# Kernel optimization log

Measured on AMD Instinct MI355X. Metric: run time of the kernel, lower is better.

The kernel has to match this reference:

```python
import jax, jax.numpy as jnp
import numpy as np

NUM_HEAD = 32
SIZE_PER_HEAD = 64
START_LEN = 4080
SEQ_LEN = 4096
STEPS = SEQ_LEN - START_LEN  # 16 unrolled decode steps
BATCH = 32
SCALE = 0.125  # hard-coded in the original (1/sqrt(64))


def setup_inputs() -> dict:
    key = jax.random.key(0)
    ks = jax.random.split(key, 7)
    B, H, D, S = BATCH, NUM_HEAD, SIZE_PER_HEAD, SEQ_LEN
    xavier = float(np.sqrt(6.0 / (D + D)))  # xavier_uniform_ bound for [D, D] fan
    return {
        "x": jax.random.normal(ks[0], (B, H, 1, D), dtype=jnp.float32),
        "k": jax.random.normal(ks[1], (B, H, S, D), dtype=jnp.float32),
        "v": jax.random.normal(ks[2], (B, H, S, D), dtype=jnp.float32),
        "wq": jax.random.uniform(ks[3], (H, D, D), jnp.float32, -xavier, xavier),
        "wk": jax.random.uniform(ks[4], (H, D, D), jnp.float32, -xavier, xavier),
        "wv": jax.random.uniform(ks[5], (H, D, D), jnp.float32, -xavier, xavier),
        "wo": jax.random.uniform(ks[6], (H, D, D), jnp.float32, -xavier, xavier),
    }


def _decode(x, k, v, wq, wk, wv, wo):
    # x: [B, H, 1, D]; k, v: [B, H, S, D]; weights: [H, D, D]
    def step(carry, _):
        x, k, v, gen_id = carry
        q = jnp.einsum("bhod,hde->bhoe", x, wq)            # [B, H, 1, D]
        k_new = jnp.einsum("bhod,hde->bhoe", x, wk)        # [B, H, 1, D]
        v_new = jnp.einsum("bhod,hde->bhoe", x, wv)
        k = jax.lax.dynamic_update_slice_in_dim(k, k_new, gen_id, axis=2)
        v = jax.lax.dynamic_update_slice_in_dim(v, v_new, gen_id, axis=2)
        # scores over the FULL cache (no mask), matching torch softmax over dim=3
        attn = jnp.einsum("bhsd,bhod->bhos", k, q) * SCALE  # [B, H, 1, S]
        attn = jax.nn.softmax(attn, axis=-1)
        x = jnp.einsum("bhos,bhsd->bhod", attn, v)          # [B, H, 1, D]
        x = jnp.einsum("bhod,hde->bhoe", x, wo)
        return (x, k, v, gen_id + 1), None

    (x, k, v, _), _ = jax.lax.scan(step, (x, k, v, jnp.int32(START_LEN)), None, length=STEPS)
    return x


def reference(x, k, v, wq, wk, wv, wo):
    return _decode(x, k, v, wq, wk, wv, wo)
```

## Files before the change

### kernel.cpp

```cpp
#include <hip/hip_runtime.h>
#include <hip/hip_fp16.h>
#include <math.h>

#define BATCH   32
#define NHEAD   32
#define DIM     64
#define SEQ     4096
#define START   4080
#define NSTEPS  16
#define SCALE   0.125f

typedef float fvec4 __attribute__((ext_vector_type(4)));

template <bool USE_WS>
__launch_bounds__(256, 6)
__global__ void attn_unroll_kernel(const float* __restrict__ x_in,
                                   const float* __restrict__ k_in,
                                   const float* __restrict__ v_in,
                                   const float* __restrict__ wq,
                                   const float* __restrict__ wk,
                                   const float* __restrict__ wv,
                                   const float* __restrict__ wo,
                                   float* __restrict__ out,
                                   __half* __restrict__ kh_ws,
                                   __half* __restrict__ vh_ws)
{
    const int bid = blockIdx.x;
    const int h   = bid & (NHEAD - 1);
    const int tid = threadIdx.x;

    __shared__ float s_scores[SEQ];
    __shared__ float s_kext[NSTEPS][DIM];
    __shared__ float s_vext[NSTEPS][DIM];
    __shared__ float s_x[DIM];
    __shared__ float s_q[DIM];
    __shared__ float s_attn[DIM];
    __shared__ float s_red[4][DIM];
    __shared__ float s_wred[4];

    const float* __restrict__ K  = k_in + (size_t)bid * SEQ * DIM;
    const float* __restrict__ V  = v_in + (size_t)bid * SEQ * DIM;
    const float* __restrict__ Wq = wq + (size_t)h * DIM * DIM;
    const float* __restrict__ Wk = wk + (size_t)h * DIM * DIM;
    const float* __restrict__ Wv = wv + (size_t)h * DIM * DIM;
    const float* __restrict__ Wo = wo + (size_t)h * DIM * DIM;
    __half* __restrict__ Kh = USE_WS ? kh_ws + (size_t)bid * START * DIM : nullptr;
    __half* __restrict__ Vh = USE_WS ? vh_ws + (size_t)bid * START * DIM : nullptr;

    if (tid < DIM) s_x[tid] = x_in[(size_t)bid * DIM + tid];
    for (int i = tid; i < NSTEPS * DIM; i += 256) {
        (&s_kext[0][0])[i] = K[(size_t)START * DIM + i];
        (&s_vext[0][0])[i] = V[(size_t)START * DIM + i];
    }
    __syncthreads();

    auto project = [&](const float* in_vec, const float* __restrict__ W,
                       float* out_vec) {
        const int e = tid & 63;
        const int g = tid >> 6;
        float p = 0.f;
        #pragma unroll
        for (int dd = 0; dd < 16; ++dd) {
            const int d0 = g * 16 + dd;
            p += in_vec[d0] * W[d0 * 64 + e];
        }
        s_red[g][e] = p;
        __syncthreads();
        if (tid < 64)
            out_vec[tid] = s_red[0][tid] + s_red[1][tid]
                         + s_red[2][tid] + s_red[3][tid];
        __syncthreads();
    };

    const int c    = tid & 15;
    const int sr   = tid >> 4;
    const int c8   = tid & 7;
    const int rg   = tid >> 3;
    const int wave = tid >> 6;

    auto qk_f32 = [&]() {
        const float q0 = s_q[c * 4 + 0], q1 = s_q[c * 4 + 1];
        const float q2 = s_q[c * 4 + 2], q3 = s_q[c * 4 + 3];
        const fvec4* __restrict__ K4 = (const fvec4*)K;
        for (int it = 0; it < START / 16; ++it) {
            const int s = it * 16 + sr;
            const fvec4 kv = __builtin_nontemporal_load(&K4[s * 16 + c]);
            if (USE_WS) {
                __half2* dst = (__half2*)(Kh + (size_t)s * DIM + c * 4);
                dst[0] = __floats2half2_rn(kv.x, kv.y);
                dst[1] = __floats2half2_rn(kv.z, kv.w);
            }
            float p = kv.x * q0 + kv.y * q1 + kv.z * q2 + kv.w * q3;
            p += __shfl_xor(p, 1);
            p += __shfl_xor(p, 2);
            p += __shfl_xor(p, 4);
            p += __shfl_xor(p, 8);
            if (c == 0) s_scores[s] = p;
        }
        {
            const int s = START + sr;
            const float* kr = s_kext[sr];
            float p = kr[c * 4 + 0] * q0 + kr[c * 4 + 1] * q1
                    + kr[c * 4 + 2] * q2 + kr[c * 4 + 3] * q3;
            p += __shfl_xor(p, 1);
            p += __shfl_xor(p, 2);
            p += __shfl_xor(p, 4);
            p += __shfl_xor(p, 8);
            if (c == 0) s_scores[s] = p;
        }
    };

    auto qk_h = [&]() {
        float qv[8];
        #pragma unroll
        for (int j = 0; j < 8; ++j) qv[j] = s_q[c8 * 8 + j];
        const fvec4* __restrict__ Kh4 = (const fvec4*)Kh;
        auto row = [&](int s) {
            fvec4 raw = Kh4[(size_t)s * 8 + c8];
            const __half2* hp = (const __half2*)&raw;
            float p = 0.f;
            #pragma unroll
            for (int j = 0; j < 4; ++j) {
                const float2 f = __half22float2(hp[j]);
                p += f.x * qv[2 * j] + f.y * qv[2 * j + 1];
            }
            p += __shfl_xor(p, 1);
            p += __shfl_xor(p, 2);
            p += __shfl_xor(p, 4);
            if (c8 == 0) s_scores[s] = p;
        };
        for (int it = 0; it < 127; ++it)
            row(it * 32 + rg);
        if (rg < 16) {
            row(4064 + rg);
            const float* kr = s_kext[rg];
            float p = 0.f;
            #pragma unroll
            for (int j = 0; j < 8; ++j) p += kr[c8 * 8 + j] * qv[j];
            p += __shfl_xor(p, 1);
            p += __shfl_xor(p, 2);
            p += __shfl_xor(p, 4);
            if (c8 == 0) s_scores[START + rg] = p;
        }
    };

    auto pv_f32 = [&](float inv_total) {
        float ax = 0.f, ay = 0.f, az = 0.f, aw = 0.f;
        const fvec4* __restrict__ V4 = (const fvec4*)V;
        for (int it = 0; it < START / 16; ++it) {
            const int s = it * 16 + sr;
            const fvec4 vv = __builtin_nontemporal_load(&V4[s * 16 + c]);
            if (USE_WS) {
                __half2* dst = (__half2*)(Vh + (size_t)s * DIM + c * 4);
                dst[0] = __floats2half2_rn(vv.x, vv.y);
                dst[1] = __floats2half2_rn(vv.z, vv.w);
            }
            const float a = s_scores[s];
            ax += a * vv.x; ay += a * vv.y; az += a * vv.z; aw += a * vv.w;
        }
        {
            const int s = START + sr;
            const float a  = s_scores[s];
            const float* vr = s_vext[sr];
            ax += a * vr[c * 4 + 0]; ay += a * vr[c * 4 + 1];
            az += a * vr[c * 4 + 2]; aw += a * vr[c * 4 + 3];
        }
        ax += __shfl_xor(ax, 16); ax += __shfl_xor(ax, 32);
        ay += __shfl_xor(ay, 16); ay += __shfl_xor(ay, 32);
        az += __shfl_xor(az, 16); az += __shfl_xor(az, 32);
        aw += __shfl_xor(aw, 16); aw += __shfl_xor(aw, 32);
        if ((tid & 63) < 16) {
            s_red[wave][c * 4 + 0] = ax;
            s_red[wave][c * 4 + 1] = ay;
            s_red[wave][c * 4 + 2] = az;
            s_red[wave][c * 4 + 3] = aw;
        }
        __syncthreads();
        if (tid < 64)
            s_attn[tid] = (s_red[0][tid] + s_red[1][tid]
                         + s_red[2][tid] + s_red[3][tid]) * inv_total;
        __syncthreads();
    };

    auto pv_h = [&](float inv_total) {
        float a[8];
        #pragma unroll
        for (int j = 0; j < 8; ++j) a[j] = 0.f;
        const fvec4* __restrict__ Vh4 = (const fvec4*)Vh;
        auto row = [&](int s) {
            const float w = s_scores[s];
            fvec4 raw = Vh4[(size_t)s * 8 + c8];
            const __half2* hp = (const __half2*)&raw;
            #pragma unroll
            for (int j = 0; j < 4; ++j) {
                const float2 f = __half22float2(hp[j]);
                a[2 * j + 0] += w * f.x;
                a[2 * j + 1] += w * f.y;
            }
        };
        for (int it = 0; it < 127; ++it)
            row(it * 32 + rg);
        if (rg < 16) {
            row(4064 + rg);
            const float w = s_scores[START + rg];
            const float* vr = s_vext[rg];
            #pragma unroll
            for (int j = 0; j < 8; ++j) a[j] += w * vr[c8 * 8 + j];
        }
        #pragma unroll
        for (int j = 0; j < 8; ++j) {
            a[j] += __shfl_xor(a[j], 8);
            a[j] += __shfl_xor(a[j], 16);
            a[j] += __shfl_xor(a[j], 32);
        }
        if ((tid & 63) < 8) {
            #pragma unroll
            for (int j = 0; j < 8; ++j) s_red[wave][c8 * 8 + j] = a[j];
        }
        __syncthreads();
        if (tid < 64)
            s_attn[tid] = (s_red[0][tid] + s_red[1][tid]
                         + s_red[2][tid] + s_red[3][tid]) * inv_total;
        __syncthreads();
    };

    for (int step = 0; step < NSTEPS; ++step) {
        project(s_x, Wq, s_q);
        project(s_x, Wk, s_kext[step]);
        project(s_x, Wv, s_vext[step]);
        if (tid < 64) s_q[tid] *= SCALE;
        __syncthreads();

        if (USE_WS && step > 0) qk_h(); else qk_f32();
        __syncthreads();

        float lmax = -1e30f;
        #pragma unroll
        for (int i = 0; i < 16; ++i)
            lmax = fmaxf(lmax, s_scores[tid + i * 256]);
        #pragma unroll
        for (int off = 1; off < 64; off <<= 1)
            lmax = fmaxf(lmax, __shfl_xor(lmax, off));
        if ((tid & 63) == 0) s_wred[wave] = lmax;
        __syncthreads();
        const float bmax = fmaxf(fmaxf(s_wred[0], s_wred[1]),
                                 fmaxf(s_wred[2], s_wred[3]));
        float lsum = 0.f;
        #pragma unroll
        for (int i = 0; i < 16; ++i) {
            const float e = __expf(s_scores[tid + i * 256] - bmax);
            s_scores[tid + i * 256] = e;
            lsum += e;
        }
        #pragma unroll
        for (int off = 1; off < 64; off <<= 1)
            lsum += __shfl_xor(lsum, off);
        __syncthreads();
        if ((tid & 63) == 0) s_wred[wave] = lsum;
        __syncthreads();
        const float inv_total = 1.f / (s_wred[0] + s_wred[1]
                                     + s_wred[2] + s_wred[3]);

        if (USE_WS && step > 0) pv_h(inv_total); else pv_f32(inv_total);

        project(s_attn, Wo, s_x);
    }

    if (tid < 64) out[(size_t)bid * DIM + tid] = s_x[tid];
}

extern "C" void kernel_launch(void* const* d_in, const int* in_sizes, int n_in,
                              void* d_out, int out_size, void* d_ws, size_t ws_size,
                              hipStream_t stream) {
    const float* x  = (const float*)d_in[0];
    const float* k  = (const float*)d_in[1];
    const float* v  = (const float*)d_in[2];
    const float* wq = (const float*)d_in[3];
    const float* wk = (const float*)d_in[4];
    const float* wv = (const float*)d_in[5];
    const float* wo = (const float*)d_in[6];
    float* out = (float*)d_out;

    const size_t half_elems = (size_t)BATCH * NHEAD * START * DIM;
    const size_t need = 2 * half_elems * sizeof(__half);

    if (ws_size >= need) {
        __half* kh = (__half*)d_ws;
        __half* vh = kh + half_elems;
        attn_unroll_kernel<true><<<BATCH * NHEAD, 256, 0, stream>>>(
            x, k, v, wq, wk, wv, wo, out, kh, vh);
    } else {
        attn_unroll_kernel<false><<<BATCH * NHEAD, 256, 0, stream>>>(
            x, k, v, wq, wk, wv, wo, out, nullptr, nullptr);
    }
}
```

Before: 3.746 ms.

## Fuse QK and PV into a single online-softmax pass over the cache

```diff
diff --git a/kernel.cpp b/kernel.cpp
--- a/kernel.cpp
+++ b/kernel.cpp
@@ -13,7 +13,7 @@
 typedef float fvec4 __attribute__((ext_vector_type(4)));
 
 template <bool USE_WS>
-__launch_bounds__(256, 6)
+__launch_bounds__(256, 4)
 __global__ void attn_unroll_kernel(const float* __restrict__ x_in,
                                    const float* __restrict__ k_in,
                                    const float* __restrict__ v_in,
@@ -29,14 +29,14 @@
     const int h   = bid & (NHEAD - 1);
     const int tid = threadIdx.x;
 
-    __shared__ float s_scores[SEQ];
     __shared__ float s_kext[NSTEPS][DIM];
     __shared__ float s_vext[NSTEPS][DIM];
     __shared__ float s_x[DIM];
     __shared__ float s_q[DIM];
     __shared__ float s_attn[DIM];
     __shared__ float s_red[4][DIM];
-    __shared__ float s_wred[4];
+    __shared__ float s_wacc[4][DIM];
+    __shared__ float s_wm[4], s_wsum[4];
 
     const float* __restrict__ K  = k_in + (size_t)bid * SEQ * DIM;
     const float* __restrict__ V  = v_in + (size_t)bid * SEQ * DIM;
@@ -72,156 +72,151 @@
         __syncthreads();
     };
 
-    const int c    = tid & 15;
-    const int sr   = tid >> 4;
     const int c8   = tid & 7;
     const int rg   = tid >> 3;
     const int wave = tid >> 6;
 
-    auto qk_f32 = [&]() {
-        const float q0 = s_q[c * 4 + 0], q1 = s_q[c * 4 + 1];
-        const float q2 = s_q[c * 4 + 2], q3 = s_q[c * 4 + 3];
+    float qv[8], acc[8], lsum, om;
+
+    auto online_row = [&](float p, const float* vv) {
+        p += __shfl_xor(p, 1);
+        p += __shfl_xor(p, 2);
+        p += __shfl_xor(p, 4);
+        float tmax = p;
+        tmax = fmaxf(tmax, __shfl_xor(tmax, 8));
+        tmax = fmaxf(tmax, __shfl_xor(tmax, 16));
+        tmax = fmaxf(tmax, __shfl_xor(tmax, 32));
+        const float mn = fmaxf(om, tmax);
+        const float f  = __expf(om - mn);
+        om = mn;
+        lsum *= f;
+        #pragma unroll
+        for (int j = 0; j < 8; ++j) acc[j] *= f;
+        const float e = __expf(p - om);
+        lsum += e;
+        #pragma unroll
+        for (int j = 0; j < 8; ++j) acc[j] += e * vv[j];
+    };
+
+    auto merge = [&]() {
+        #pragma unroll
+        for (int j = 0; j < 8; ++j) {
+            acc[j] += __shfl_xor(acc[j], 8);
+            acc[j] += __shfl_xor(acc[j], 16);
+            acc[j] += __shfl_xor(acc[j], 32);
+        }
+        lsum += __shfl_xor(lsum, 8);
+        lsum += __shfl_xor(lsum, 16);
+        lsum += __shfl_xor(lsum, 32);
+        if ((tid & 63) == 0) { s_wm[wave] = om; s_wsum[wave] = lsum; }
+        if ((tid & 63) < 8) {
+            #pragma unroll
+            for (int j = 0; j < 8; ++j) s_wacc[wave][c8 * 8 + j] = acc[j];
+        }
+        __syncthreads();
+        if (tid < 64) {
+            const float M = fmaxf(fmaxf(s_wm[0], s_wm[1]),
+                                  fmaxf(s_wm[2], s_wm[3]));
+            float tot = 0.f, val = 0.f;
+            #pragma unroll
+            for (int w = 0; w < 4; ++w) {
+                const float f = __expf(s_wm[w] - M);
+                tot += s_wsum[w] * f;
+                val += s_wacc[w][tid] * f;
+            }
+            s_attn[tid] = val / tot;
+        }
+        __syncthreads();
+    };
+
+    auto ext_rows = [&]() {
+        if (wave < 2) {
+            const float* kr = s_kext[rg];
+            const float* vr = s_vext[rg];
+            float p = 0.f;
+            #pragma unroll
+            for (int j = 0; j < 8; ++j) p += kr[c8 * 8 + j] * qv[j];
+            float vv[8];
+            #pragma unroll
+            for (int j = 0; j < 8; ++j) vv[j] = vr[c8 * 8 + j];
+            online_row(p, vv);
+        }
+    };
+
+    auto pass_f32 = [&]() {
+        #pragma unroll
+        for (int j = 0; j < 8; ++j) qv[j] = s_q[c8 * 8 + j];
+        #pragma unroll
+        for (int j = 0; j < 8; ++j) acc[j] = 0.f;
+        lsum = 0.f; om = -1e30f;
         const fvec4* __restrict__ K4 = (const fvec4*)K;
-        for (int it = 0; it < START / 16; ++it) {
-            const int s = it * 16 + sr;
-            const fvec4 kv = __builtin_nontemporal_load(&K4[s * 16 + c]);
+        const fvec4* __restrict__ V4 = (const fvec4*)V;
+        auto row = [&](int s) {
+            const fvec4 ka = K4[(size_t)s * 16 + 2 * c8];
+            const fvec4 kb = K4[(size_t)s * 16 + 2 * c8 + 1];
+            const fvec4 va = V4[(size_t)s * 16 + 2 * c8];
+            const fvec4 vb = V4[(size_t)s * 16 + 2 * c8 + 1];
             if (USE_WS) {
-                __half2* dst = (__half2*)(Kh + (size_t)s * DIM + c * 4);
-                dst[0] = __floats2half2_rn(kv.x, kv.y);
-                dst[1] = __floats2half2_rn(kv.z, kv.w);
-            }
-            float p = kv.x * q0 + kv.y * q1 + kv.z * q2 + kv.w * q3;
-            p += __shfl_xor(p, 1);
-            p += __shfl_xor(p, 2);
-            p += __shfl_xor(p, 4);
-            p += __shfl_xor(p, 8);
-            if (c == 0) s_scores[s] = p;
-        }
-        {
-            const int s = START + sr;
-            const float* kr = s_kext[sr];
-            float p = kr[c * 4 + 0] * q0 + kr[c * 4 + 1] * q1
-                    + kr[c * 4 + 2] * q2 + kr[c * 4 + 3] * q3;
-            p += __shfl_xor(p, 1);
-            p += __shfl_xor(p, 2);
-            p += __shfl_xor(p, 4);
-            p += __shfl_xor(p, 8);
-            if (c == 0) s_scores[s] = p;
-        }
-    };
-
-    auto qk_h = [&]() {
-        float qv[8];
-        #pragma unroll
-        for (int j = 0; j < 8; ++j) qv[j] = s_q[c8 * 8 + j];
-        const fvec4* __restrict__ Kh4 = (const fvec4*)Kh;
-        auto row = [&](int s) {
-            fvec4 raw = Kh4[(size_t)s * 8 + c8];
-            const __half2* hp = (const __half2*)&raw;
-            float p = 0.f;
-            #pragma unroll
-            for (int j = 0; j < 4; ++j) {
-                const float2 f = __half22float2(hp[j]);
-                p += f.x * qv[2 * j] + f.y * qv[2 * j + 1];
-            }
-            p += __shfl_xor(p, 1);
-            p += __shfl_xor(p, 2);
-            p += __shfl_xor(p, 4);
-            if (c8 == 0) s_scores[s] = p;
+                union { fvec4 v; __half2 hh[4]; } uk, uv;
+                uk.hh[0] = __floats2half2_rn(ka.x, ka.y);
+                uk.hh[1] = __floats2half2_rn(ka.z, ka.w);
+                uk.hh[2] = __floats2half2_rn(kb.x, kb.y);
+                uk.hh[3] = __floats2half2_rn(kb.z, kb.w);
+                uv.hh[0] = __floats2half2_rn(va.x, va.y);
+                uv.hh[1] = __floats2half2_rn(va.z, va.w);
+                uv.hh[2] = __floats2half2_rn(vb.x, vb.y);
+                uv.hh[3] = __floats2half2_rn(vb.z, vb.w);
+                *(fvec4*)(Kh + (size_t)s * DIM + c8 * 8) = uk.v;
+                *(fvec4*)(Vh + (size_t)s * DIM + c8 * 8) = uv.v;
+            }
+            float p = ka.x * qv[0] + ka.y * qv[1] + ka.z * qv[2] + ka.w * qv[3]
+                    + kb.x * qv[4] + kb.y * qv[5] + kb.z * qv[6] + kb.w * qv[7];
+            const float vv[8] = { va.x, va.y, va.z, va.w,
+                                  vb.x, vb.y, vb.z, vb.w };
+            online_row(p, vv);
         };
         for (int it = 0; it < 127; ++it)
             row(it * 32 + rg);
-        if (rg < 16) {
+        if (wave < 2)
             row(4064 + rg);
-            const float* kr = s_kext[rg];
-            float p = 0.f;
-            #pragma unroll
-            for (int j = 0; j < 8; ++j) p += kr[c8 * 8 + j] * qv[j];
-            p += __shfl_xor(p, 1);
-            p += __shfl_xor(p, 2);
-            p += __shfl_xor(p, 4);
-            if (c8 == 0) s_scores[START + rg] = p;
-        }
-    };
-
-    auto pv_f32 = [&](float inv_total) {
-        float ax = 0.f, ay = 0.f, az = 0.f, aw = 0.f;
-        const fvec4* __restrict__ V4 = (const fvec4*)V;
-        for (int it = 0; it < START / 16; ++it) {
-            const int s = it * 16 + sr;
-            const fvec4 vv = __builtin_nontemporal_load(&V4[s * 16 + c]);
-            if (USE_WS) {
-                __half2* dst = (__half2*)(Vh + (size_t)s * DIM + c * 4);
-                dst[0] = __floats2half2_rn(vv.x, vv.y);
-                dst[1] = __floats2half2_rn(vv.z, vv.w);
-            }
-            const float a = s_scores[s];
-            ax += a * vv.x; ay += a * vv.y; az += a * vv.z; aw += a * vv.w;
-        }
-        {
-            const int s = START + sr;
-            const float a  = s_scores[s];
-            const float* vr = s_vext[sr];
-            ax += a * vr[c * 4 + 0]; ay += a * vr[c * 4 + 1];
-            az += a * vr[c * 4 + 2]; aw += a * vr[c * 4 + 3];
-        }
-        ax += __shfl_xor(ax, 16); ax += __shfl_xor(ax, 32);
-        ay += __shfl_xor(ay, 16); ay += __shfl_xor(ay, 32);
-        az += __shfl_xor(az, 16); az += __shfl_xor(az, 32);
-        aw += __shfl_xor(aw, 16); aw += __shfl_xor(aw, 32);
-        if ((tid & 63) < 16) {
-            s_red[wave][c * 4 + 0] = ax;
-            s_red[wave][c * 4 + 1] = ay;
-            s_red[wave][c * 4 + 2] = az;
-            s_red[wave][c * 4 + 3] = aw;
-        }
-        __syncthreads();
-        if (tid < 64)
-            s_attn[tid] = (s_red[0][tid] + s_red[1][tid]
-                         + s_red[2][tid] + s_red[3][tid]) * inv_total;
-        __syncthreads();
-    };
-
-    auto pv_h = [&](float inv_total) {
-        float a[8];
-        #pragma unroll
-        for (int j = 0; j < 8; ++j) a[j] = 0.f;
+        ext_rows();
+        merge();
+    };
+
+    auto pass_h = [&]() {
+        #pragma unroll
+        for (int j = 0; j < 8; ++j) qv[j] = s_q[c8 * 8 + j];
+        #pragma unroll
+        for (int j = 0; j < 8; ++j) acc[j] = 0.f;
+        lsum = 0.f; om = -1e30f;
+        const fvec4* __restrict__ Kh4 = (const fvec4*)Kh;
         const fvec4* __restrict__ Vh4 = (const fvec4*)Vh;
         auto row = [&](int s) {
-            const float w = s_scores[s];
-            fvec4 raw = Vh4[(size_t)s * 8 + c8];
-            const __half2* hp = (const __half2*)&raw;
+            fvec4 kraw = Kh4[(size_t)s * 8 + c8];
+            fvec4 vraw = Vh4[(size_t)s * 8 + c8];
+            const __half2* kp = (const __half2*)&kraw;
+            const __half2* vp = (const __half2*)&vraw;
+            float p = 0.f;
             #pragma unroll
             for (int j = 0; j < 4; ++j) {
-                const float2 f = __half22float2(hp[j]);
-                a[2 * j + 0] += w * f.x;
-                a[2 * j + 1] += w * f.y;
-            }
+                const float2 f = __half22float2(kp[j]);
+                p += f.x * qv[2 * j] + f.y * qv[2 * j + 1];
+            }
+            float vv[8];
+            #pragma unroll
+            for (int j = 0; j < 4; ++j) {
+                const float2 f = __half22float2(vp[j]);
+                vv[2 * j + 0] = f.x;
+                vv[2 * j + 1] = f.y;
+            }
+            online_row(p, vv);
         };
         for (int it = 0; it < 127; ++it)
             row(it * 32 + rg);
-        if (rg < 16) {
+        if (wave < 2)
             row(4064 + rg);
-            const float w = s_scores[START + rg];
-            const float* vr = s_vext[rg];
-            #pragma unroll
-            for (int j = 0; j < 8; ++j) a[j] += w * vr[c8 * 8 + j];
-        }
-        #pragma unroll
-        for (int j = 0; j < 8; ++j) {
-            a[j] += __shfl_xor(a[j], 8);
-            a[j] += __shfl_xor(a[j], 16);
-            a[j] += __shfl_xor(a[j], 32);
-        }
-        if ((tid & 63) < 8) {
-            #pragma unroll
-            for (int j = 0; j < 8; ++j) s_red[wave][c8 * 8 + j] = a[j];
-        }
-        __syncthreads();
-        if (tid < 64)
-            s_attn[tid] = (s_red[0][tid] + s_red[1][tid]
-                         + s_red[2][tid] + s_red[3][tid]) * inv_total;
-        __syncthreads();
+        ext_rows();
+        merge();
     };
 
     for (int step = 0; step < NSTEPS; ++step) {
@@ -231,37 +226,7 @@
         if (tid < 64) s_q[tid] *= SCALE;
         __syncthreads();
 
-        if (USE_WS && step > 0) qk_h(); else qk_f32();
-        __syncthreads();
-
-        float lmax = -1e30f;
-        #pragma unroll
-        for (int i = 0; i < 16; ++i)
-            lmax = fmaxf(lmax, s_scores[tid + i * 256]);
-        #pragma unroll
-        for (int off = 1; off < 64; off <<= 1)
-            lmax = fmaxf(lmax, __shfl_xor(lmax, off));
-        if ((tid & 63) == 0) s_wred[wave] = lmax;
-        __syncthreads();
-        const float bmax = fmaxf(fmaxf(s_wred[0], s_wred[1]),
-                                 fmaxf(s_wred[2], s_wred[3]));
-        float lsum = 0.f;
-        #pragma unroll
-        for (int i = 0; i < 16; ++i) {
-            const float e = __expf(s_scores[tid + i * 256] - bmax);
-            s_scores[tid + i * 256] = e;
-            lsum += e;
-        }
-        #pragma unroll
-        for (int off = 1; off < 64; off <<= 1)
-            lsum += __shfl_xor(lsum, off);
-        __syncthreads();
-        if ((tid & 63) == 0) s_wred[wave] = lsum;
-        __syncthreads();
-        const float inv_total = 1.f / (s_wred[0] + s_wred[1]
-                                     + s_wred[2] + s_wred[3]);
-
-        if (USE_WS && step > 0) pv_h(inv_total); else pv_f32(inv_total);
+        if (USE_WS && step > 0) pass_h(); else pass_f32();
 
         project(s_attn, Wo, s_x);
     }
```

Measured after the change: 3.329 ms. -11.1%, faster.
